# Kernel tuning notes

Measured on AMD Instinct MI355X. Metric: run time of the kernel, lower is better.

The kernel has to match this reference:

```python
import jax, jax.numpy as jnp
import numpy as np

L, B, T, C, H = 8, 2, 1024, 1024, 16
DH = C // H          # 64, head dim (even, required for RoPE)
DFF = 4 * C          # 4096
THETA = 10000.0
EPS = 1e-5


def _ln(x, scale, bias):
    m = jnp.mean(x, axis=-1, keepdims=True)
    v = jnp.mean((x - m) ** 2, axis=-1, keepdims=True)
    return (x - m) * jax.lax.rsqrt(v + EPS) * scale + bias


def _rope_cos_sin():
    # matches precompute_freqs_cis: freqs_cis[t, j] = exp(i * t * theta^{-2j/dim})
    inv = 1.0 / (THETA ** (jnp.arange(0, DH, 2, dtype=jnp.float32) / DH))  # (DH/2,)
    ang = jnp.arange(T, dtype=jnp.float32)[:, None] * inv[None, :]         # (T, DH/2)
    return jnp.cos(ang), jnp.sin(ang)


def _apply_rope(x, cos, sin):
    # x: (B,H,T,DH); complex multiply on interleaved pairs == torch.view_as_complex path
    xr = x.reshape(B, H, T, DH // 2, 2)
    x0, x1 = xr[..., 0], xr[..., 1]
    o0 = x0 * cos - x1 * sin
    o1 = x0 * sin + x1 * cos
    return jnp.stack([o0, o1], axis=-1).reshape(B, H, T, DH)


def setup_inputs() -> dict:
    key = jax.random.key(0)
    ks = jax.random.split(key, 20)
    s = 0.02
    p = lambda k, shape: (jax.random.normal(k, shape, jnp.float32) * s)
    return {
        "x": jax.random.normal(ks[0], (B, T, C), jnp.float32),
        "Wq": p(ks[1], (L, C, C)), "bq": jnp.zeros((L, C), jnp.float32),
        "Wk": p(ks[2], (L, C, C)), "bk": jnp.zeros((L, C), jnp.float32),
        "Wv": p(ks[3], (L, C, C)), "bv": jnp.zeros((L, C), jnp.float32),
        "Wo": p(ks[4], (L, C, C)), "bo": jnp.zeros((L, C), jnp.float32),
        "ln1_s": jnp.ones((L, C), jnp.float32), "ln1_b": jnp.zeros((L, C), jnp.float32),
        "ln2_s": jnp.ones((L, C), jnp.float32), "ln2_b": jnp.zeros((L, C), jnp.float32),
        "W1": p(ks[5], (L, C, DFF)), "b1": jnp.zeros((L, DFF), jnp.float32),
        "W2": p(ks[6], (L, DFF, C)), "b2": jnp.zeros((L, C), jnp.float32),
        "lnf_s": jnp.ones((C,), jnp.float32), "lnf_b": jnp.zeros((C,), jnp.float32),
    }


def reference(x, Wq, bq, Wk, bk, Wv, bv, Wo, bo,
              ln1_s, ln1_b, ln2_s, ln2_b, W1, b1, W2, b2, lnf_s, lnf_b):
    cos, sin = _rope_cos_sin()
    causal = jnp.tril(jnp.ones((T, T), bool))
    inv_sqrt_dh = jnp.float32(1.0 / np.sqrt(DH))

    def layer(h, p):
        wq, bq_, wk, bk_, wv, bv_, wo, bo_, s1, c1, s2, c2, w1, d1, w2, d2 = p
        a = _ln(h, s1, c1)
        q = (a @ wq + bq_).reshape(B, T, H, DH).transpose(0, 2, 1, 3)  # (B,H,T,DH)
        k = (a @ wk + bk_).reshape(B, T, H, DH).transpose(0, 2, 1, 3)
        v = (a @ wv + bv_).reshape(B, T, H, DH).transpose(0, 2, 1, 3)
        q = _apply_rope(q, cos, sin)
        k = _apply_rope(k, cos, sin)
        att = jnp.einsum('bhqd,bhkd->bhqk', q, k) * inv_sqrt_dh
        att = jnp.where(causal, att, -jnp.inf)
        att = jax.nn.softmax(att, axis=-1)
        y = jnp.einsum('bhqk,bhkd->bhqd', att, v)
        y = y.transpose(0, 2, 1, 3).reshape(B, T, C)
        h = h + (y @ wo + bo_)
        m = _ln(h, s2, c2)
        h = h + (jax.nn.gelu(m @ w1 + d1, approximate=False) @ w2 + d2)
        return h, None

    h, _ = jax.lax.scan(
        layer, x,
        (Wq, bq, Wk, bk, Wv, bv, Wo, bo, ln1_s, ln1_b, ln2_s, ln2_b, W1, b1, W2, b2))
    return _ln(h, lnf_s, lnf_b)
```

## Files before the change

kernel.cpp:

```cpp
#include <hip/hip_runtime.h>
#include <cstdint>
#include <cstddef>

#define L_   8
#define B_   2
#define T_   1024
#define C_   1024
#define H_   16
#define DH_  64
#define DFF_ 4096
#define M_   2048

typedef __attribute__((ext_vector_type(4))) float f32x4;
typedef __attribute__((ext_vector_type(8))) short short8_t;
typedef __attribute__((ext_vector_type(8))) __bf16 bf16x8_t;
typedef __attribute__((ext_vector_type(4))) unsigned short ushort4_t;

__device__ __forceinline__ float bf2f(unsigned short u) {
  unsigned int i = ((unsigned int)u) << 16;
  return __builtin_bit_cast(float, i);
}
__device__ __forceinline__ unsigned short f2bf(float f) {
  unsigned int u = __builtin_bit_cast(unsigned int, f);
  u += 0x7fff + ((u >> 16) & 1);
  return (unsigned short)(u >> 16);
}
__device__ __forceinline__ f32x4 mfma16x16x32(short8_t a, short8_t b, f32x4 c) {
  return __builtin_amdgcn_mfma_f32_16x16x32_bf16(
      __builtin_bit_cast(bf16x8_t, a), __builtin_bit_cast(bf16x8_t, b), c, 0, 0, 0);
}
__device__ __forceinline__ void async_copy16(const void* g, void* l) {
  __builtin_amdgcn_global_load_lds(
      (const __attribute__((address_space(1))) unsigned int*)g,
      (__attribute__((address_space(3))) unsigned int*)l, 16, 0, 0);
}

__global__ __launch_bounds__(256) void convert_k(
    const float* __restrict__ Wq, const float* __restrict__ Wk,
    const float* __restrict__ Wv, const float* __restrict__ Wo,
    const float* __restrict__ W1, const float* __restrict__ W2,
    unsigned short* __restrict__ wt) {
  __shared__ float tile[32][33];
  const int bx = blockIdx.x;
  const int layer = bx / 12288;
  const int r = bx - layer * 12288;
  const float* src; unsigned short* dst; int R, Cc, t;
  unsigned short* wl = wt + (size_t)layer * 12582912;
  if (r < 3072) {
    const int mat = r >> 10; t = r & 1023;
    src = (mat == 0 ? Wq : mat == 1 ? Wk : Wv) + (size_t)layer * 1048576;
    dst = wl + (size_t)mat * 1048576; R = 1024; Cc = 1024;
  } else if (r < 4096) {
    t = r - 3072; src = Wo + (size_t)layer * 1048576;
    dst = wl + 3145728; R = 1024; Cc = 1024;
  } else if (r < 8192) {
    t = r - 4096; src = W1 + (size_t)layer * 4194304;
    dst = wl + 4194304; R = 1024; Cc = 4096;
  } else {
    t = r - 8192; src = W2 + (size_t)layer * 4194304;
    dst = wl + 8388608; R = 4096; Cc = 1024;
  }
  const int nTc = Cc >> 5;
  const int tr = t / nTc, tc = t - tr * nTc;
  const int r0 = tr * 32, c0 = tc * 32;
  const int tx = threadIdx.x & 31, ty = threadIdx.x >> 5;
#pragma unroll
  for (int i = 0; i < 4; ++i)
    tile[ty + 8*i][tx] = src[(size_t)(r0 + ty + 8*i) * Cc + c0 + tx];
  __syncthreads();
#pragma unroll
  for (int i = 0; i < 4; ++i)
    dst[(size_t)(c0 + ty + 8*i) * R + r0 + tx] = f2bf(tile[tx][ty + 8*i]);
}

__global__ __launch_bounds__(256) void ln_k(const float* __restrict__ X,
                                            const float* __restrict__ gam,
                                            const float* __restrict__ bet,
                                            unsigned short* __restrict__ out) {
  const int row = blockIdx.x;
  const int tid = threadIdx.x;
  const int lane = tid & 63, w = tid >> 6;
  const float4 v = ((const float4*)(X + (size_t)row * C_))[tid];
  float sum = v.x + v.y + v.z + v.w;
  float sq  = v.x*v.x + v.y*v.y + v.z*v.z + v.w*v.w;
#pragma unroll
  for (int d = 1; d < 64; d <<= 1) {
    sum += __shfl_xor(sum, d, 64);
    sq  += __shfl_xor(sq,  d, 64);
  }
  __shared__ float red[8];
  if (lane == 0) { red[w] = sum; red[4 + w] = sq; }
  __syncthreads();
  sum = red[0] + red[1] + red[2] + red[3];
  sq  = red[4] + red[5] + red[6] + red[7];
  const float mean = sum * (1.0f / C_);
  const float var  = sq * (1.0f / C_) - mean * mean;
  const float inv  = rsqrtf(var + 1e-5f);
  const int col = tid * 4;
  const float xs[4] = { v.x, v.y, v.z, v.w };
  ushort4_t ov;
#pragma unroll
  for (int i = 0; i < 4; ++i)
    ov[i] = f2bf((xs[i]-mean)*inv*gam[col+i] + bet[col+i]);
  *(ushort4_t*)(out + (size_t)row * C_ + col) = ov;
}

template<int NS, int FINAL>
__global__ __launch_bounds__(256) void reduce_ln(
    float* __restrict__ h, const float* __restrict__ bias,
    const float* __restrict__ part,
    const float* __restrict__ gam, const float* __restrict__ bet,
    void* __restrict__ out) {
  const int row = blockIdx.x;
  const int tid = threadIdx.x;
  const int lane = tid & 63, w = tid >> 6;
  const size_t base = (size_t)row * C_;
  float4 v = ((const float4*)(h + base))[tid];
  const float4 b = ((const float4*)bias)[tid];
  v.x += b.x; v.y += b.y; v.z += b.z; v.w += b.w;
#pragma unroll
  for (int z = 0; z < NS; ++z) {
    const float4 p = ((const float4*)(part + (size_t)z * M_ * C_ + base))[tid];
    v.x += p.x; v.y += p.y; v.z += p.z; v.w += p.w;
  }
  if (!FINAL) ((float4*)(h + base))[tid] = v;
  float sum = v.x + v.y + v.z + v.w;
  float sq  = v.x*v.x + v.y*v.y + v.z*v.z + v.w*v.w;
#pragma unroll
  for (int d = 1; d < 64; d <<= 1) {
    sum += __shfl_xor(sum, d, 64);
    sq  += __shfl_xor(sq,  d, 64);
  }
  __shared__ float red[8];
  if (lane == 0) { red[w] = sum; red[4 + w] = sq; }
  __syncthreads();
  sum = red[0] + red[1] + red[2] + red[3];
  sq  = red[4] + red[5] + red[6] + red[7];
  const float mean = sum * (1.0f / C_);
  const float var  = sq * (1.0f / C_) - mean * mean;
  const float inv  = rsqrtf(var + 1e-5f);
  const float4 g  = ((const float4*)gam)[tid];
  const float4 be = ((const float4*)bet)[tid];
  if (FINAL) {
    float4 ov;
    ov.x = (v.x-mean)*inv*g.x + be.x;
    ov.y = (v.y-mean)*inv*g.y + be.y;
    ov.z = (v.z-mean)*inv*g.z + be.z;
    ov.w = (v.w-mean)*inv*g.w + be.w;
    ((float4*)out)[(size_t)row * 256 + tid] = ov;
  } else {
    ushort4_t ov;
    const float xs[4] = { v.x, v.y, v.z, v.w };
    const float gs[4] = { g.x, g.y, g.z, g.w };
    const float bs[4] = { be.x, be.y, be.z, be.w };
#pragma unroll
    for (int i = 0; i < 4; ++i)
      ov[i] = f2bf((xs[i]-mean)*inv*gs[i] + bs[i]);
    *(ushort4_t*)((unsigned short*)out + base + tid * 4) = ov;
  }
}

template<int EPI>
__global__ __launch_bounds__(256) void gemm64(
    const unsigned short* __restrict__ A,
    const unsigned short* __restrict__ Bt,
    const float* __restrict__ bias0,
    const float* __restrict__ bias1,
    const float* __restrict__ bias2,
    void* __restrict__ out0, void* __restrict__ out1, void* __restrict__ out2,
    int M, int N, int K) {
  __shared__ __align__(16) unsigned short As[64 * 32];
  __shared__ __align__(16) unsigned short Bs[128 * 32];
  const int tid = threadIdx.x;
  const int lane = tid & 63;
  const int w = tid >> 6;
  const int ln15 = lane & 15, lg = lane >> 4;
  const int row0 = blockIdx.y * 64, col0 = blockIdx.x * 128;
  const int wr = w >> 1, wc = w & 1;

  const int kper = K / gridDim.z;
  const int k0 = blockIdx.z * kper;

  f32x4 acc[2][4] = {};

  const int rA  = tid >> 2,          ccA = (tid & 3) * 8;
  const int rB0 = tid >> 2,          ccB = (tid & 3) * 8;
  const int rB1 = (256 + tid) >> 2;

  for (int kt = k0; kt < k0 + kper; kt += 32) {
    async_copy16(A  + (size_t)(row0 + rA)  * K + kt + ccA, (char*)As + ((size_t)w * 64) * 16);
    async_copy16(Bt + (size_t)(col0 + rB0) * K + kt + ccB, (char*)Bs + ((size_t)w * 64) * 16);
    async_copy16(Bt + (size_t)(col0 + rB1) * K + kt + ccB, (char*)Bs + ((size_t)(256 + w * 64)) * 16);
    __syncthreads();
    short8_t af[2], bfr[4];
#pragma unroll
    for (int m = 0; m < 2; ++m)
      af[m] = *(const short8_t*)(As + (wr*32 + m*16 + ln15) * 32 + lg * 8);
#pragma unroll
    for (int n = 0; n < 4; ++n)
      bfr[n] = *(const short8_t*)(Bs + (wc*64 + n*16 + ln15) * 32 + lg * 8);
#pragma unroll
    for (int m = 0; m < 2; ++m)
#pragma unroll
      for (int n = 0; n < 4; ++n)
        acc[m][n] = mfma16x16x32(af[m], bfr[n], acc[m][n]);
    __syncthreads();
  }

#pragma unroll
  for (int m = 0; m < 2; ++m) {
#pragma unroll
    for (int n = 0; n < 4; ++n) {
#pragma unroll
      for (int r = 0; r < 4; ++r) {
        const int rg = row0 + wr*32 + m*16 + lg*4 + r;
        const int cg = col0 + wc*64 + n*16 + ln15;
        float v = acc[m][n][r];
        if (EPI == 0) {
          if (cg < 2048) {
            v += (cg < 1024) ? bias0[cg] : bias1[cg - 1024];
            const float vp = __shfl_xor(v, 1, 64);
            const int j = (cg & 63) >> 1;
            const float ang = (float)(rg & 1023) *
                              exp2f((float)j * -0.41524101186092029f);
            float sn, cs;
            sincosf(ang, &sn, &cs);
            const float ov = (cg & 1) ? (vp * sn + v * cs) : (v * cs - vp * sn);
            unsigned short* dstp = (cg < 1024) ? (unsigned short*)out0
                                               : (unsigned short*)out1;
            dstp[(size_t)rg * C_ + (cg & 1023)] = f2bf(ov);
          } else {
            const int ch = cg - 2048;
            v += bias2[ch];
            const int hh = ch >> 6, dh = ch & 63;
            const int bb = rg >> 10, t = rg & 1023;
            ((unsigned short*)out2)[(((size_t)(bb * H_ + hh) * DH_ + dh) << 10) + t] = f2bf(v);
          }
        } else {
          ((float*)out0)[((size_t)blockIdx.z * M_ + rg) * (size_t)N + cg] = v;
        }
      }
    }
  }
}

__global__ __launch_bounds__(256) void gemm128_gelu(
    const unsigned short* __restrict__ A,
    const unsigned short* __restrict__ Bt,
    const float* __restrict__ bias,
    unsigned short* __restrict__ out,
    int M, int N, int K) {
  __shared__ __align__(16) unsigned short As[128 * 32];
  __shared__ __align__(16) unsigned short Bs[128 * 32];
  const int tid = threadIdx.x;
  const int lane = tid & 63;
  const int w = tid >> 6;
  const int ln15 = lane & 15, lg = lane >> 4;
  const int row0 = blockIdx.y * 128, col0 = blockIdx.x * 128;
  const int wr = w >> 1, wc = w & 1;

  f32x4 acc[4][4] = {};

  const int r0s = tid >> 2,         cc0 = (tid & 3) * 8;
  const int r1s = (256 + tid) >> 2, cc1 = (tid & 3) * 8;

  for (int kt = 0; kt < K; kt += 32) {
    async_copy16(A  + (size_t)(row0 + r0s) * K + kt + cc0, (char*)As + ((size_t)w * 64) * 16);
    async_copy16(A  + (size_t)(row0 + r1s) * K + kt + cc1, (char*)As + ((size_t)(256 + w * 64)) * 16);
    async_copy16(Bt + (size_t)(col0 + r0s) * K + kt + cc0, (char*)Bs + ((size_t)w * 64) * 16);
    async_copy16(Bt + (size_t)(col0 + r1s) * K + kt + cc1, (char*)Bs + ((size_t)(256 + w * 64)) * 16);
    __syncthreads();
    short8_t af[4], bfr[4];
#pragma unroll
    for (int m = 0; m < 4; ++m)
      af[m] = *(const short8_t*)(As + (wr*64 + m*16 + ln15) * 32 + lg * 8);
#pragma unroll
    for (int n = 0; n < 4; ++n)
      bfr[n] = *(const short8_t*)(Bs + (wc*64 + n*16 + ln15) * 32 + lg * 8);
#pragma unroll
    for (int m = 0; m < 4; ++m)
#pragma unroll
      for (int n = 0; n < 4; ++n)
        acc[m][n] = mfma16x16x32(af[m], bfr[n], acc[m][n]);
    __syncthreads();
  }

#pragma unroll
  for (int m = 0; m < 4; ++m) {
#pragma unroll
    for (int n = 0; n < 4; ++n) {
#pragma unroll
      for (int r = 0; r < 4; ++r) {
        const int rg = row0 + wr*64 + m*16 + lg*4 + r;
        const int cg = col0 + wc*64 + n*16 + ln15;
        float v = acc[m][n][r] + bias[cg];
        v = 0.5f * v * (1.0f + erff(v * 0.70710678118654752f));
        out[(size_t)rg * N + cg] = f2bf(v);
      }
    }
  }
}

template<bool MASK>
__device__ __forceinline__ void attn_tile(
    const int kb, const int ln15, const int lg, const int rowg0,
    const unsigned short* __restrict__ Kp,
    const unsigned short* __restrict__ Vp,
    const short8_t aq0, const short8_t aq1,
    float* __restrict__ m_run, float* __restrict__ l_run,
    f32x4* __restrict__ o, unsigned short* __restrict__ P) {
  const unsigned short* kt = Kp + (size_t)kb * 64 * C_;
  const unsigned short* vt = Vp + kb * 64;
  short8_t bk[4][2], vb[2][4];
#pragma unroll
  for (int n = 0; n < 4; ++n) {
    bk[n][0] = *(const short8_t*)(kt + (size_t)n * 16 * C_);
    bk[n][1] = *(const short8_t*)(kt + (size_t)n * 16 * C_ + 32);
  }
  f32x4 s[4] = {};
#pragma unroll
  for (int n = 0; n < 4; ++n) {
    s[n] = mfma16x16x32(aq0, bk[n][0], s[n]);
    s[n] = mfma16x16x32(aq1, bk[n][1], s[n]);
  }
#pragma unroll
  for (int c = 0; c < 2; ++c)
#pragma unroll
    for (int n = 0; n < 4; ++n)
      vb[c][n] = *(const short8_t*)(vt + (size_t)n * 16 * T_ + c * 32);

  const float SCL = 0.18033688011116012f;
  float mx[4];
#pragma unroll
  for (int r = 0; r < 4; ++r) {
    float mr = -1e30f;
#pragma unroll
    for (int n = 0; n < 4; ++n) {
      float v = s[n][r] * SCL;
      if (MASK && (kb * 64 + n * 16 + ln15) > (rowg0 + r)) v = -1e30f;
      s[n][r] = v;
      mr = fmaxf(mr, v);
    }
    mx[r] = mr;
  }
#pragma unroll
  for (int d = 1; d < 16; d <<= 1)
#pragma unroll
    for (int r = 0; r < 4; ++r) mx[r] = fmaxf(mx[r], __shfl_xor(mx[r], d, 64));
#pragma unroll
  for (int r = 0; r < 4; ++r) {
    const float mn = fmaxf(m_run[r], mx[r]);
    const float scf = exp2f(m_run[r] - mn);
    m_run[r] = mn;
    float rs = 0.0f;
#pragma unroll
    for (int n = 0; n < 4; ++n) {
      const float pv = exp2f(s[n][r] - mn);
      s[n][r] = pv;
      rs += pv;
    }
#pragma unroll
    for (int d = 1; d < 16; d <<= 1) rs += __shfl_xor(rs, d, 64);
    l_run[r] = l_run[r] * scf + rs;
#pragma unroll
    for (int n = 0; n < 4; ++n) o[n][r] *= scf;
  }
  __syncthreads();
#pragma unroll
  for (int r = 0; r < 4; ++r)
#pragma unroll
    for (int n = 0; n < 4; ++n)
      P[(lg * 4 + r) * 64 + n * 16 + ln15] = f2bf(s[n][r]);
  __syncthreads();
#pragma unroll
  for (int c = 0; c < 2; ++c) {
    const short8_t pa = *(const short8_t*)(P + ln15 * 64 + c * 32 + lg * 8);
#pragma unroll
    for (int n = 0; n < 4; ++n)
      o[n] = mfma16x16x32(pa, vb[c][n], o[n]);
  }
}

__global__ __launch_bounds__(64) void attn_k(const unsigned short* __restrict__ Q,
                                             const unsigned short* __restrict__ Kb,
                                             const unsigned short* __restrict__ Vt,
                                             unsigned short* __restrict__ Y) {
  __shared__ __align__(16) unsigned short P[16 * 64];
  const int lane = threadIdx.x;
  const int ln15 = lane & 15, lg = lane >> 4;
  const int qt = blockIdx.x, bh = blockIdx.y;
  const int b = bh >> 4, h = bh & 15;
  const int q0 = qt * 16;

  short8_t aq0, aq1;
  {
    const unsigned short* qp = Q + ((size_t)(b * T_ + q0 + ln15)) * C_ + h * DH_ + lg * 8;
    aq0 = *(const short8_t*)(qp);
    aq1 = *(const short8_t*)(qp + 32);
  }
  float m_run[4] = { -1e30f, -1e30f, -1e30f, -1e30f };
  float l_run[4] = {};
  f32x4 o[4] = {};
  const int rowg0 = q0 + lg * 4;
  const unsigned short* Kp = Kb + ((size_t)b * T_ + ln15) * C_ + h * DH_ + lg * 8;
  const unsigned short* Vp = Vt + ((size_t)bh * DH_ + ln15) * T_ + lg * 8;

  const int kb_last = qt >> 2;
  for (int kb = 0; kb < kb_last; ++kb)
    attn_tile<false>(kb, ln15, lg, rowg0, Kp, Vp, aq0, aq1, m_run, l_run, o, P);
  attn_tile<true>(kb_last, ln15, lg, rowg0, Kp, Vp, aq0, aq1, m_run, l_run, o, P);

#pragma unroll
  for (int n = 0; n < 4; ++n)
#pragma unroll
    for (int r = 0; r < 4; ++r) {
      const float val = o[n][r] / l_run[r];
      Y[((size_t)(b * T_ + rowg0 + r)) * C_ + h * DH_ + n * 16 + ln15] = f2bf(val);
    }
}

extern "C" void kernel_launch(void* const* d_in, const int* in_sizes, int n_in,
                              void* d_out, int out_size, void* d_ws, size_t ws_size,
                              hipStream_t stream) {
  const float* x    = (const float*)d_in[0];
  const float* Wq   = (const float*)d_in[1];
  const float* bq   = (const float*)d_in[2];
  const float* Wk   = (const float*)d_in[3];
  const float* bk   = (const float*)d_in[4];
  const float* Wv   = (const float*)d_in[5];
  const float* bv   = (const float*)d_in[6];
  const float* Wo   = (const float*)d_in[7];
  const float* bo   = (const float*)d_in[8];
  const float* ln1s = (const float*)d_in[9];
  const float* ln1b = (const float*)d_in[10];
  const float* ln2s = (const float*)d_in[11];
  const float* ln2b = (const float*)d_in[12];
  const float* W1   = (const float*)d_in[13];
  const float* b1   = (const float*)d_in[14];
  const float* W2   = (const float*)d_in[15];
  const float* b2   = (const float*)d_in[16];
  const float* lnfs = (const float*)d_in[17];
  const float* lnfb = (const float*)d_in[18];

  const size_t MB = (size_t)1 << 20;
  char* ws = (char*)d_ws;
  float*          h      = (float*)(ws + 0);
  unsigned short* a_bf   = (unsigned short*)(ws + 8*MB);
  unsigned short* q_bf   = (unsigned short*)(ws + 12*MB);
  unsigned short* k_bf   = (unsigned short*)(ws + 16*MB);
  unsigned short* vt_bf  = (unsigned short*)(ws + 20*MB);
  unsigned short* y_bf   = (unsigned short*)(ws + 24*MB);
  unsigned short* mid_bf = (unsigned short*)(ws + 28*MB);
  float*          part   = (float*)(ws + 44*MB);
  unsigned short* wt_all = (unsigned short*)(ws + 76*MB);

  convert_k<<<8 * 12288, 256, 0, stream>>>(Wq, Wk, Wv, Wo, W1, W2, wt_all);
  hipMemcpyAsync(h, x, (size_t)M_ * C_ * sizeof(float), hipMemcpyDeviceToDevice, stream);
  ln_k<<<M_, 256, 0, stream>>>(h, ln1s, ln1b, a_bf);

  for (int l = 0; l < L_; ++l) {
    const unsigned short* wt_l = wt_all + (size_t)l * 12582912;
    gemm64<0><<<dim3(24, 32, 1), 256, 0, stream>>>(a_bf, wt_l,
        bq + l*C_, bk + l*C_, bv + l*C_, q_bf, k_bf, vt_bf, M_, 3*C_, C_);
    attn_k<<<dim3(T_/16, B_*H_), 64, 0, stream>>>(q_bf, k_bf, vt_bf, y_bf);
    gemm64<3><<<dim3(8, 32, 2), 256, 0, stream>>>(y_bf, wt_l + 3145728,
        nullptr, nullptr, nullptr, part, nullptr, nullptr, M_, C_, C_);
    reduce_ln<2, 0><<<M_, 256, 0, stream>>>(h, bo + l*C_, part,
        ln2s + l*C_, ln2b + l*C_, a_bf);
    gemm128_gelu<<<dim3(32, 16), 256, 0, stream>>>(a_bf, wt_l + 4194304,
        b1 + l*DFF_, mid_bf, M_, DFF_, C_);
    gemm64<3><<<dim3(8, 32, 4), 256, 0, stream>>>(mid_bf, wt_l + 8388608,
        nullptr, nullptr, nullptr, part, nullptr, nullptr, M_, C_, DFF_);
    if (l < L_ - 1) {
      reduce_ln<4, 0><<<M_, 256, 0, stream>>>(h, b2 + l*C_, part,
          ln1s + (l+1)*C_, ln1b + (l+1)*C_, a_bf);
    } else {
      reduce_ln<4, 1><<<M_, 256, 0, stream>>>(h, b2 + l*C_, part,
          lnfs, lnfb, d_out);
    }
  }
}
```

Before: 1.859 ms.

## Widen weight-transpose tiles and double attention key block to 128

The weight conversion kernel now transposes 64x64 tiles, reading with float4 loads and writing eight bf16 values per store, with a quarter as many blocks. The attention kernel processes 128 keys per tile instead of 64, which halves the number of softmax rescale and barrier rounds per query tile and uses a padded P buffer stride. The larger key tile raises register use (8 score accumulators, 16 V fragments) and, for the diagonal tile, does more masked work that is thrown away.

Measured after the change: 1.853 ms. About the same (-0.4%).

```diff
diff --git a/kernel.cpp b/kernel.cpp
--- a/kernel.cpp
+++ b/kernel.cpp
@@ -15,6 +15,7 @@
 typedef __attribute__((ext_vector_type(8))) short short8_t;
 typedef __attribute__((ext_vector_type(8))) __bf16 bf16x8_t;
 typedef __attribute__((ext_vector_type(4))) unsigned short ushort4_t;
+typedef __attribute__((ext_vector_type(8))) unsigned short ushort8_t;
 
 __device__ __forceinline__ float bf2f(unsigned short u) {
   unsigned int i = ((unsigned int)u) << 16;
@@ -40,37 +41,48 @@
     const float* __restrict__ Wv, const float* __restrict__ Wo,
     const float* __restrict__ W1, const float* __restrict__ W2,
     unsigned short* __restrict__ wt) {
-  __shared__ float tile[32][33];
+  __shared__ float tile[64][68];
   const int bx = blockIdx.x;
-  const int layer = bx / 12288;
-  const int r = bx - layer * 12288;
+  const int layer = bx / 3072;
+  const int r = bx - layer * 3072;
   const float* src; unsigned short* dst; int R, Cc, t;
   unsigned short* wl = wt + (size_t)layer * 12582912;
-  if (r < 3072) {
-    const int mat = r >> 10; t = r & 1023;
+  if (r < 768) {
+    const int mat = r >> 8; t = r & 255;
     src = (mat == 0 ? Wq : mat == 1 ? Wk : Wv) + (size_t)layer * 1048576;
     dst = wl + (size_t)mat * 1048576; R = 1024; Cc = 1024;
-  } else if (r < 4096) {
-    t = r - 3072; src = Wo + (size_t)layer * 1048576;
+  } else if (r < 1024) {
+    t = r - 768; src = Wo + (size_t)layer * 1048576;
     dst = wl + 3145728; R = 1024; Cc = 1024;
-  } else if (r < 8192) {
-    t = r - 4096; src = W1 + (size_t)layer * 4194304;
+  } else if (r < 2048) {
+    t = r - 1024; src = W1 + (size_t)layer * 4194304;
     dst = wl + 4194304; R = 1024; Cc = 4096;
   } else {
-    t = r - 8192; src = W2 + (size_t)layer * 4194304;
+    t = r - 2048; src = W2 + (size_t)layer * 4194304;
     dst = wl + 8388608; R = 4096; Cc = 1024;
   }
-  const int nTc = Cc >> 5;
+  const int nTc = Cc >> 6;
   const int tr = t / nTc, tc = t - tr * nTc;
-  const int r0 = tr * 32, c0 = tc * 32;
-  const int tx = threadIdx.x & 31, ty = threadIdx.x >> 5;
-#pragma unroll
-  for (int i = 0; i < 4; ++i)
-    tile[ty + 8*i][tx] = src[(size_t)(r0 + ty + 8*i) * Cc + c0 + tx];
+  const int r0 = tr * 64, c0 = tc * 64;
+  const int tid = threadIdx.x;
+  const int tx = tid & 15, ty = tid >> 4;
+#pragma unroll
+  for (int i = 0; i < 4; ++i) {
+    const int row = ty + 16 * i;
+    const float4 v = *(const float4*)(src + (size_t)(r0 + row) * Cc + c0 + tx * 4);
+    *(float4*)&tile[row][tx * 4] = v;
+  }
   __syncthreads();
 #pragma unroll
-  for (int i = 0; i < 4; ++i)
-    dst[(size_t)(c0 + ty + 8*i) * R + r0 + tx] = f2bf(tile[tx][ty + 8*i]);
+  for (int pass = 0; pass < 2; ++pass) {
+    const int chunk = pass * 256 + tid;
+    const int c = chunk >> 3;
+    const int off = (chunk & 7) * 8;
+    ushort8_t val;
+#pragma unroll
+    for (int j = 0; j < 8; ++j) val[j] = f2bf(tile[off + j][c]);
+    *(ushort8_t*)(dst + (size_t)(c0 + c) * R + r0 + off) = val;
+  }
 }
 
 __global__ __launch_bounds__(256) void ln_k(const float* __restrict__ X,
@@ -301,6 +313,8 @@
   }
 }
 
+#define PSTR 136
+
 template<bool MASK>
 __device__ __forceinline__ void attn_tile(
     const int kb, const int ln15, const int lg, const int rowg0,
@@ -309,22 +323,20 @@
     const short8_t aq0, const short8_t aq1,
     float* __restrict__ m_run, float* __restrict__ l_run,
     f32x4* __restrict__ o, unsigned short* __restrict__ P) {
-  const unsigned short* kt = Kp + (size_t)kb * 64 * C_;
-  const unsigned short* vt = Vp + kb * 64;
-  short8_t bk[4][2], vb[2][4];
-#pragma unroll
-  for (int n = 0; n < 4; ++n) {
-    bk[n][0] = *(const short8_t*)(kt + (size_t)n * 16 * C_);
-    bk[n][1] = *(const short8_t*)(kt + (size_t)n * 16 * C_ + 32);
-  }
-  f32x4 s[4] = {};
-#pragma unroll
-  for (int n = 0; n < 4; ++n) {
-    s[n] = mfma16x16x32(aq0, bk[n][0], s[n]);
-    s[n] = mfma16x16x32(aq1, bk[n][1], s[n]);
-  }
-#pragma unroll
-  for (int c = 0; c < 2; ++c)
+  const unsigned short* kt = Kp + (size_t)kb * 128 * C_;
+  const unsigned short* vt = Vp + kb * 128;
+  f32x4 s[8];
+#pragma unroll
+  for (int n = 0; n < 8; ++n) {
+    const short8_t b0 = *(const short8_t*)(kt + (size_t)n * 16 * C_);
+    const short8_t b1 = *(const short8_t*)(kt + (size_t)n * 16 * C_ + 32);
+    f32x4 z = {};
+    z = mfma16x16x32(aq0, b0, z);
+    s[n] = mfma16x16x32(aq1, b1, z);
+  }
+  short8_t vb[4][4];
+#pragma unroll
+  for (int c = 0; c < 4; ++c)
 #pragma unroll
     for (int n = 0; n < 4; ++n)
       vb[c][n] = *(const short8_t*)(vt + (size_t)n * 16 * T_ + c * 32);
@@ -335,9 +347,9 @@
   for (int r = 0; r < 4; ++r) {
     float mr = -1e30f;
 #pragma unroll
-    for (int n = 0; n < 4; ++n) {
+    for (int n = 0; n < 8; ++n) {
       float v = s[n][r] * SCL;
-      if (MASK && (kb * 64 + n * 16 + ln15) > (rowg0 + r)) v = -1e30f;
+      if (MASK && (kb * 128 + n * 16 + ln15) > (rowg0 + r)) v = -1e30f;
       s[n][r] = v;
       mr = fmaxf(mr, v);
     }
@@ -354,7 +366,7 @@
     m_run[r] = mn;
     float rs = 0.0f;
 #pragma unroll
-    for (int n = 0; n < 4; ++n) {
+    for (int n = 0; n < 8; ++n) {
       const float pv = exp2f(s[n][r] - mn);
       s[n][r] = pv;
       rs += pv;
@@ -369,12 +381,12 @@
 #pragma unroll
   for (int r = 0; r < 4; ++r)
 #pragma unroll
-    for (int n = 0; n < 4; ++n)
-      P[(lg * 4 + r) * 64 + n * 16 + ln15] = f2bf(s[n][r]);
+    for (int n = 0; n < 8; ++n)
+      P[(lg * 4 + r) * PSTR + n * 16 + ln15] = f2bf(s[n][r]);
   __syncthreads();
 #pragma unroll
-  for (int c = 0; c < 2; ++c) {
-    const short8_t pa = *(const short8_t*)(P + ln15 * 64 + c * 32 + lg * 8);
+  for (int c = 0; c < 4; ++c) {
+    const short8_t pa = *(const short8_t*)(P + ln15 * PSTR + c * 32 + lg * 8);
 #pragma unroll
     for (int n = 0; n < 4; ++n)
       o[n] = mfma16x16x32(pa, vb[c][n], o[n]);
@@ -385,7 +397,7 @@
                                              const unsigned short* __restrict__ Kb,
                                              const unsigned short* __restrict__ Vt,
                                              unsigned short* __restrict__ Y) {
-  __shared__ __align__(16) unsigned short P[16 * 64];
+  __shared__ __align__(16) unsigned short P[16 * PSTR];
   const int lane = threadIdx.x;
   const int ln15 = lane & 15, lg = lane >> 4;
   const int qt = blockIdx.x, bh = blockIdx.y;
@@ -405,7 +417,7 @@
   const unsigned short* Kp = Kb + ((size_t)b * T_ + ln15) * C_ + h * DH_ + lg * 8;
   const unsigned short* Vp = Vt + ((size_t)bh * DH_ + ln15) * T_ + lg * 8;
 
-  const int kb_last = qt >> 2;
+  const int kb_last = qt >> 3;
   for (int kb = 0; kb < kb_last; ++kb)
     attn_tile<false>(kb, ln15, lg, rowg0, Kp, Vp, aq0, aq1, m_run, l_run, o, P);
   attn_tile<true>(kb_last, ln15, lg, rowg0, Kp, Vp, aq0, aq1, m_run, l_run, o, P);
@@ -454,7 +466,7 @@
   float*          part   = (float*)(ws + 44*MB);
   unsigned short* wt_all = (unsigned short*)(ws + 76*MB);
 
-  convert_k<<<8 * 12288, 256, 0, stream>>>(Wq, Wk, Wv, Wo, W1, W2, wt_all);
+  convert_k<<<8 * 3072, 256, 0, stream>>>(Wq, Wk, Wv, Wo, W1, W2, wt_all);
   hipMemcpyAsync(h, x, (size_t)M_ * C_ * sizeof(float), hipMemcpyDeviceToDevice, stream);
   ln_k<<<M_, 256, 0, stream>>>(h, ln1s, ln1b, a_bf);
 
```
